# Performance work log

Measured on AMD Instinct MI355X. Metric: run time of the kernel, lower is better.

The kernel has to match this reference:

```python
import jax, jax.numpy as jnp
import numpy as np

D = 1024
H = 16
HD = D // H
LN_EPS = 1e-5
RMS_EPS = 1e-6


def layernorm(x, g, b):
    mu = jnp.mean(x, axis=-1, keepdims=True)
    var = jnp.mean(jnp.square(x - mu), axis=-1, keepdims=True)
    return (x - mu) * jax.lax.rsqrt(var + LN_EPS) * g + b


def rmsnorm(x, w):
    ms = jnp.mean(jnp.square(x), axis=-1, keepdims=True)
    return x * jax.lax.rsqrt(ms + RMS_EPS) * w


def setup_inputs() -> dict:
    key = jax.random.key(0)
    ks = jax.random.split(key, 8)
    s = 0.02
    ones = jnp.ones((D,), jnp.float32)
    zeros = jnp.zeros((D,), jnp.float32)
    return {
        "query_tokens": jax.random.normal(ks[0], (4, 512, D), jnp.float32),
        "point_features": jax.random.normal(ks[1], (4, 4096, D), jnp.float32),
        "ln_q_g": ones, "ln_q_b": zeros,
        "ln_kv_g": ones, "ln_kv_b": zeros,
        "Wq": jax.random.normal(ks[2], (D, D), jnp.float32) * s, "bq": zeros,
        "Wk": jax.random.normal(ks[3], (D, D), jnp.float32) * s, "bk": zeros,
        "Wv": jax.random.normal(ks[4], (D, D), jnp.float32) * s, "bv": zeros,
        "rms_q_w": ones, "rms_k_w": ones,
        "Wo": jax.random.normal(ks[5], (D, D), jnp.float32) * s, "bo": zeros,
        "ln_mlp_g": ones, "ln_mlp_b": zeros,
        "W1": jax.random.normal(ks[6], (D, 4 * D), jnp.float32) * s,
        "b1": jnp.zeros((4 * D,), jnp.float32),
        "W2": jax.random.normal(ks[7], (4 * D, D), jnp.float32) * s,
        "b2": zeros,
    }


def reference(query_tokens, point_features, ln_q_g, ln_q_b, ln_kv_g, ln_kv_b,
              Wq, bq, Wk, bk, Wv, bv, rms_q_w, rms_k_w, Wo, bo,
              ln_mlp_g, ln_mlp_b, W1, b1, W2, b2):
    B, K, _ = query_tokens.shape
    N = point_features.shape[1]
    q_in = layernorm(query_tokens, ln_q_g, ln_q_b)
    kv_in = layernorm(point_features, ln_kv_g, ln_kv_b)
    q = rmsnorm(q_in @ Wq + bq, rms_q_w)          # [B,K,D]
    k = rmsnorm(kv_in @ Wk + bk, rms_k_w)         # [B,N,D]
    v = kv_in @ Wv + bv                            # [B,N,D]
    q = q.reshape(B, K, H, HD)
    k = k.reshape(B, N, H, HD)
    v = v.reshape(B, N, H, HD)
    scores = jnp.einsum('bkhd,bnhd->bhkn', q, k) / jnp.sqrt(jnp.float32(HD))
    attn = jax.nn.softmax(scores, axis=-1)
    ctx = jnp.einsum('bhkn,bnhd->bkhd', attn, v).reshape(B, K, D)
    out = ctx @ Wo + bo + query_tokens
    h = layernorm(out, ln_mlp_g, ln_mlp_b)
    mlp = jax.nn.gelu(h @ W1 + b1, approximate=False) @ W2 + b2
    return out + mlp
```

## Files before the change

### kernel.cpp

```cpp
#include <hip/hip_runtime.h>
#include <math.h>

#define DD   1024
#define NHD  16
#define HDIM 64
#define BB   4
#define QN   512
#define KVN  4096
#define FF   4096

typedef __attribute__((ext_vector_type(8))) short bf16x8;
typedef __attribute__((ext_vector_type(4))) float f32x4;

__device__ __forceinline__ float b2f(ushort u){
  union { unsigned u32; float f; } x; x.u32 = ((unsigned)u)<<16; return x.f;
}
__device__ __forceinline__ ushort f2b(float f){
  unsigned u = __float_as_uint(f);
  unsigned r = (u + 0x7FFFu + ((u>>16)&1u)) >> 16;
  return (ushort)r;
}
__device__ __forceinline__ float ldx(const void* p, size_t i, int isbf){
  return isbf ? b2f(((const ushort*)p)[i]) : ((const float*)p)[i];
}
__device__ __forceinline__ int detect_bf(const void* gref){
  return ((const unsigned*)gref)[0] == 0x3F803F80u;
}

#if defined(__has_builtin)
#if __has_builtin(__builtin_amdgcn_global_load_lds)
#define HAS_GLL 1
#endif
#endif
#ifndef HAS_GLL
#define HAS_GLL 0
#endif
__device__ __forceinline__ void stage16(const ushort* g, ushort* lds_base, int lane){
#if HAS_GLL
  __builtin_amdgcn_global_load_lds(g, lds_base, 16, 0, 0);
#else
  *(uint4*)(lds_base + lane*8) = *(const uint4*)g;
#endif
}

__device__ __forceinline__ void wave_barrier(){
  asm volatile("" ::: "memory");
  __builtin_amdgcn_s_barrier();
  asm volatile("" ::: "memory");
}

__global__ __launch_bounds__(256)
void trans_all(const void* __restrict__ Wq, const void* __restrict__ Wk,
               const void* __restrict__ Wv, const void* __restrict__ Wo,
               const void* __restrict__ W1, const void* __restrict__ W2,
               ushort* __restrict__ WqT, ushort* __restrict__ WkvT,
               ushort* __restrict__ WoT,
               ushort* __restrict__ W1T, ushort* __restrict__ W2T,
               const void* __restrict__ gref)
{
  const int isbf = detect_bf(gref);
  int bid = blockIdx.x;
  const void* src; ushort* dst; int R, C, tid;
  if (bid < 1024){
    int s = bid >> 8; tid = bid & 255; R = 1024; C = 1024;
    src = (s==0) ? Wq : (s==1) ? Wk : (s==2) ? Wv : Wo;
    dst = (s==0) ? WqT : (s==1) ? WkvT : (s==2) ? (WkvT + (size_t)1024*1024) : WoT;
  } else if (bid < 2048){ tid = bid - 1024; src = W1; dst = W1T; R = 1024; C = 4096; }
  else                  { tid = bid - 2048; src = W2; dst = W2T; R = 4096; C = 1024; }
  int ntx = C >> 6;
  int tx = tid % ntx, ty = tid / ntx;
  int r0 = ty*64, c0 = tx*64;

  __shared__ __align__(16) ushort tile[64][72];
  int t = threadIdx.x;
  if (isbf){
    #pragma unroll
    for (int i=0;i<2;i++){
      int idx = t + i*256;
      int r = idx>>3, ch = idx&7;
      #pragma unroll
      for (int j=0;j<8;j++)
        tile[r][ch*8+j] = ((const ushort*)src)[(size_t)(r0+r)*C + c0 + ch*8 + j];
    }
  } else {
    #pragma unroll
    for (int i=0;i<2;i++){
      int idx = t + i*256;
      int r = idx>>3, ch = idx&7;
      const float* s4 = (const float*)src + (size_t)(r0+r)*C + c0 + ch*8;
      float4 f0 = *(const float4*)s4;
      float4 f1 = *(const float4*)(s4+4);
      tile[r][ch*8+0]=f2b(f0.x); tile[r][ch*8+1]=f2b(f0.y);
      tile[r][ch*8+2]=f2b(f0.z); tile[r][ch*8+3]=f2b(f0.w);
      tile[r][ch*8+4]=f2b(f1.x); tile[r][ch*8+5]=f2b(f1.y);
      tile[r][ch*8+6]=f2b(f1.z); tile[r][ch*8+7]=f2b(f1.w);
    }
  }
  __syncthreads();
  #pragma unroll
  for (int i=0;i<2;i++){
    int idx = t + i*256;
    int c = idx>>3, ch = idx&7;
    __align__(16) ushort tmp[8];
    #pragma unroll
    for (int j=0;j<8;j++) tmp[j] = tile[ch*8+j][c];
    *(uint4*)(dst + (size_t)(c0+c)*R + r0 + ch*8) = *(uint4*)tmp;
  }
}

__global__ __launch_bounds__(256)
void ln_all(const void* __restrict__ qtok, const void* __restrict__ pfeat,
            const void* __restrict__ gq, const void* __restrict__ bq,
            const void* __restrict__ gkv, const void* __restrict__ bkv,
            ushort* __restrict__ q_ln, ushort* __restrict__ kv_ln,
            const void* __restrict__ gref)
{
  const int isbf = detect_bf(gref);
  int row = blockIdx.x, t = threadIdx.x;
  const void* src; const void* g; const void* bb; ushort* dst; int r;
  if (row < BB*QN){ src = qtok;  g = gq;  bb = bq;  dst = q_ln;  r = row; }
  else            { src = pfeat; g = gkv; bb = bkv; dst = kv_ln; r = row - BB*QN; }
  int c0 = t*4;
  float v[4];
  if (isbf){
    #pragma unroll
    for (int i=0;i<4;i++) v[i] = b2f(((const ushort*)src)[(size_t)r*DD + c0 + i]);
  } else {
    float4 f = *(const float4*)((const float*)src + (size_t)r*DD + c0);
    v[0]=f.x; v[1]=f.y; v[2]=f.z; v[3]=f.w;
  }
  float s1=0.f, s2=0.f;
  #pragma unroll
  for (int i=0;i<4;i++){ s1 += v[i]; s2 += v[i]*v[i]; }
  #pragma unroll
  for (int off=32; off; off>>=1){ s1 += __shfl_xor(s1,off,64); s2 += __shfl_xor(s2,off,64); }
  __shared__ float r1[4], r2[4];
  int wave = t>>6;
  if ((t&63)==0){ r1[wave]=s1; r2[wave]=s2; }
  __syncthreads();
  s1 = r1[0]+r1[1]+r1[2]+r1[3];
  s2 = r2[0]+r2[1]+r2[2]+r2[3];
  float mu  = s1 * (1.0f/DD);
  float var = s2 * (1.0f/DD) - mu*mu;
  float rs  = rsqrtf(var + 1e-5f);
  union { ushort u[4]; uint2 w; } pk;
  #pragma unroll
  for (int i=0;i<4;i++)
    pk.u[i] = f2b((v[i]-mu)*rs*ldx(g,c0+i,isbf) + ldx(bb,c0+i,isbf));
  *(uint2*)(dst + (size_t)r*DD + c0) = pk.w;
}

__global__ __launch_bounds__(256)
void ln_combine(const float* __restrict__ p0, const float* __restrict__ p1,
                const void* __restrict__ bo, const void* __restrict__ qtok,
                const void* __restrict__ g, const void* __restrict__ bb,
                float* __restrict__ outb, ushort* __restrict__ y,
                const void* __restrict__ gref)
{
  const int isbf = detect_bf(gref);
  int row = blockIdx.x, t = threadIdx.x;
  int c0 = t*4;
  size_t base = (size_t)row*DD + c0;
  float4 a0 = *(const float4*)(p0 + base);
  float4 a1 = *(const float4*)(p1 + base);
  float v[4] = {a0.x+a1.x, a0.y+a1.y, a0.z+a1.z, a0.w+a1.w};
  if (isbf){
    #pragma unroll
    for (int i=0;i<4;i++)
      v[i] += b2f(((const ushort*)qtok)[base+i]) + b2f(((const ushort*)bo)[c0+i]);
  } else {
    float4 q4 = *(const float4*)((const float*)qtok + base);
    v[0] += q4.x + ((const float*)bo)[c0+0];
    v[1] += q4.y + ((const float*)bo)[c0+1];
    v[2] += q4.z + ((const float*)bo)[c0+2];
    v[3] += q4.w + ((const float*)bo)[c0+3];
  }
  float4 ov; ov.x=v[0]; ov.y=v[1]; ov.z=v[2]; ov.w=v[3];
  *(float4*)(outb + base) = ov;

  float s1=0.f, s2=0.f;
  #pragma unroll
  for (int i=0;i<4;i++){ s1 += v[i]; s2 += v[i]*v[i]; }
  #pragma unroll
  for (int off=32; off; off>>=1){ s1 += __shfl_xor(s1,off,64); s2 += __shfl_xor(s2,off,64); }
  __shared__ float r1[4], r2[4];
  int wave = t>>6;
  if ((t&63)==0){ r1[wave]=s1; r2[wave]=s2; }
  __syncthreads();
  s1 = r1[0]+r1[1]+r1[2]+r1[3];
  s2 = r2[0]+r2[1]+r2[2]+r2[3];
  float mu  = s1 * (1.0f/DD);
  float var = s2 * (1.0f/DD) - mu*mu;
  float rs  = rsqrtf(var + 1e-5f);
  union { ushort u[4]; uint2 w; } pk;
  #pragma unroll
  for (int i=0;i<4;i++)
    pk.u[i] = f2b((v[i]-mu)*rs*ldx(g,c0+i,isbf) + ldx(bb,c0+i,isbf));
  *(uint2*)(y + base) = pk.w;
}

__global__ __launch_bounds__(256)
void combine_w2(const float* __restrict__ P0, const float* __restrict__ P1,
                const float* __restrict__ P2, const void* __restrict__ b2,
                const float* __restrict__ res, void* __restrict__ out,
                const void* __restrict__ gref)
{
  const int isbf = detect_bf(gref);
  const size_t PSZ = (size_t)BB*QN*DD;
  size_t i = ((size_t)blockIdx.x*256 + threadIdx.x)*4;
  float4 v = *(const float4*)(P0 + i);
  #pragma unroll
  for (int z=1; z<4; z++){
    float4 p = *(const float4*)(P0 + (size_t)z*PSZ + i);
    v.x+=p.x; v.y+=p.y; v.z+=p.z; v.w+=p.w;
  }
  #pragma unroll
  for (int z=0; z<2; z++){
    float4 p = *(const float4*)(P1 + (size_t)z*PSZ + i);
    v.x+=p.x; v.y+=p.y; v.z+=p.z; v.w+=p.w;
  }
  #pragma unroll
  for (int z=0; z<2; z++){
    float4 p = *(const float4*)(P2 + (size_t)z*PSZ + i);
    v.x+=p.x; v.y+=p.y; v.z+=p.z; v.w+=p.w;
  }
  float4 r = *(const float4*)(res + i);
  int col = (int)(i & (DD-1));
  v.x += r.x + ldx(b2,col+0,isbf);
  v.y += r.y + ldx(b2,col+1,isbf);
  v.z += r.z + ldx(b2,col+2,isbf);
  v.w += r.w + ldx(b2,col+3,isbf);
  if (isbf){
    union { ushort u[4]; uint2 w; } pk;
    pk.u[0]=f2b(v.x); pk.u[1]=f2b(v.y); pk.u[2]=f2b(v.z); pk.u[3]=f2b(v.w);
    *(uint2*)((ushort*)out + i) = pk.w;
  } else {
    *(float4*)((float*)out + i) = v;
  }
}

__global__ __launch_bounds__(256)
void rms_all(ushort* __restrict__ qb, const void* __restrict__ wq,
             ushort* __restrict__ kb, const void* __restrict__ wk,
             const void* __restrict__ gref)
{
  const int isbf = detect_bf(gref);
  int row = blockIdx.x, t = threadIdx.x;
  ushort* x; const void* w; int r;
  if (row < BB*QN){ x = qb; w = wq; r = row; }
  else            { x = kb; w = wk; r = row - BB*QN; }
  int c0 = t*4;
  union { ushort u[4]; uint2 w; } in;
  in.w = *(const uint2*)(x + (size_t)r*DD + c0);
  float v[4];
  #pragma unroll
  for (int i=0;i<4;i++) v[i] = b2f(in.u[i]);
  float s2 = 0.f;
  #pragma unroll
  for (int i=0;i<4;i++) s2 += v[i]*v[i];
  #pragma unroll
  for (int off=32; off; off>>=1) s2 += __shfl_xor(s2,off,64);
  __shared__ float r2[4];
  int wave = t>>6;
  if ((t&63)==0) r2[wave]=s2;
  __syncthreads();
  s2 = r2[0]+r2[1]+r2[2]+r2[3];
  float rs = rsqrtf(s2*(1.0f/DD) + 1e-6f);
  union { ushort u[4]; uint2 w; } pk;
  #pragma unroll
  for (int i=0;i<4;i++) pk.u[i] = f2b(v[i]*rs*ldx(w,c0+i,isbf));
  *(uint2*)(x + (size_t)r*DD + c0) = pk.w;
}

template<int ACT_GELU, int OUT_MODE, int RES_MODE>
__global__ __launch_bounds__(256)
void gemm_bt(const ushort* __restrict__ A, const ushort* __restrict__ BT,
             const void* __restrict__ bias,
             const void* __restrict__ res_ext, const float* __restrict__ res_f,
             void* __restrict__ Cout, void* __restrict__ Cout2,
             int M, int N, int Kdim, int Kstride,
             const void* __restrict__ gref)
{
  const int isbf = detect_bf(gref);
  __shared__ __align__(16) ushort As[128*64];
  __shared__ __align__(16) ushort Bs[128*64];
  const int bm = blockIdx.y * 128;
  const int bn = blockIdx.x * 128;
  const int kz = blockIdx.z;
  const int t = threadIdx.x;
  const int wave = t>>6, lane = t&63, quad = lane>>4, l16 = lane&15;
  const int wm = (wave&1)*64, wn = (wave>>1)*64;

  const ushort* ga[4]; const ushort* gb[4];
  #pragma unroll
  for (int j=0;j<4;j++){
    int row = (t>>3) + j*32;
    int g = ((t&7) - row) & 7;
    ga[j] = A  + (size_t)(bm+row)*Kstride + kz*Kdim + g*8;
    gb[j] = BT + (size_t)(bn+row)*Kstride + kz*Kdim + g*8;
  }

  int offA[2][4], offB[2][4];
  #pragma unroll
  for (int kk=0;kk<2;kk++)
    #pragma unroll
    for (int i=0;i<4;i++){
      int ra = wm + i*16 + l16;
      offA[kk][i] = ra*64 + ((quad + kk*4 + ra)&7)*8;
      int rb = wn + i*16 + l16;
      offB[kk][i] = rb*64 + ((quad + kk*4 + rb)&7)*8;
    }

  f32x4 zero = {0.f,0.f,0.f,0.f};
  f32x4 acc[4][4];
  #pragma unroll
  for (int i=0;i<4;i++)
    #pragma unroll
    for (int j=0;j<4;j++) acc[i][j] = zero;

  const int kiters = Kdim >> 6;
  for (int ki = 0; ki < kiters; ki++) {
    #pragma unroll
    for (int j=0;j<4;j++){
      stage16(ga[j], As + (size_t)(j*256 + wave*64)*8, lane);
      stage16(gb[j], Bs + (size_t)(j*256 + wave*64)*8, lane);
      ga[j] += 64; gb[j] += 64;
    }
    __syncthreads();
    #pragma unroll
    for (int kk=0;kk<2;kk++){
      bf16x8 af[4], bfr[4];
      #pragma unroll
      for (int i=0;i<4;i++){
        af[i]  = *(const bf16x8*)(As + offA[kk][i]);
        bfr[i] = *(const bf16x8*)(Bs + offB[kk][i]);
      }
      #pragma unroll
      for (int mt=0;mt<4;mt++)
        #pragma unroll
        for (int nt=0;nt<4;nt++)
          acc[mt][nt] = __builtin_amdgcn_mfma_f32_16x16x32_bf16(af[mt], bfr[nt], acc[mt][nt], 0,0,0);
    }
    __syncthreads();
  }

  if (OUT_MODE == 4){
    float* P = (float*)Cout + (size_t)kz*M*N;
    #pragma unroll
    for (int mt=0;mt<4;mt++){
      #pragma unroll
      for (int r=0;r<4;r++){
        int row = bm + wm + mt*16 + quad*4 + r;
        #pragma unroll
        for (int nt=0;nt<4;nt++){
          int col = bn + wn + nt*16 + l16;
          P[(size_t)row*N + col] = acc[mt][nt][r];
        }
      }
    }
    return;
  }

  float bv[4];
  #pragma unroll
  for (int nt=0;nt<4;nt++) bv[nt] = ldx(bias, bn + wn + nt*16 + l16, isbf);
  #pragma unroll
  for (int mt=0;mt<4;mt++){
    #pragma unroll
    for (int r=0;r<4;r++){
      int row = bm + wm + mt*16 + quad*4 + r;
      #pragma unroll
      for (int nt=0;nt<4;nt++){
        int col = bn + wn + nt*16 + l16;
        float v = acc[mt][nt][r] + bv[nt];
        if (ACT_GELU) v = 0.5f*v*(1.0f + erff(v*0.70710678118f));
        size_t oi = (size_t)row*N + col;
        if (RES_MODE==1) v += ldx(res_ext, oi, isbf);
        if (RES_MODE==2) v += res_f[oi];
        if (OUT_MODE==0)      ((ushort*)Cout)[oi] = f2b(v);
        else if (OUT_MODE==1) ((float*)Cout)[oi]  = v;
        else { if (isbf) ((ushort*)Cout)[oi] = f2b(v); else ((float*)Cout)[oi] = v; }
      }
    }
  }
}

#define G_HB  32768
#define G_RA0 0
#define G_RA1 8192
#define G_RB0 16384
#define G_RB1 24576

#define G_STAGE(src, R, tile) do{ \
  ushort* _d = ldsb + (((tile)&1)*G_HB + (R) + wave*1024); \
  stage16(src[0] + ((tile)<<6), _d,       lane); \
  stage16(src[1] + ((tile)<<6), _d + 512, lane); \
}while(0)

#define G_LDA(dst, base) \
  _Pragma("unroll") for (int kk=0;kk<2;kk++) \
  _Pragma("unroll") for (int m=0;m<4;m++) \
    dst[kk][m] = *(const bf16x8*)((base) + offA[kk][m]);

#define G_LDB(dst, base) \
  _Pragma("unroll") for (int kk=0;kk<2;kk++) \
  _Pragma("unroll") for (int n=0;n<2;n++) \
    dst[kk][n] = *(const bf16x8*)((base) + offB[kk][n]);

#define G_MM16(ar, br, MO, NO) \
  _Pragma("unroll") for (int kk=0;kk<2;kk++) \
  _Pragma("unroll") for (int m=0;m<4;m++) \
  _Pragma("unroll") for (int n=0;n<2;n++) \
    acc[m+(MO)][n+(NO)] = __builtin_amdgcn_mfma_f32_16x16x32_bf16(ar[kk][m], br[kk][n], acc[m+(MO)][n+(NO)], 0,0,0);

#define G_SYNC() do{ wave_barrier(); \
  asm volatile("s_waitcnt lgkmcnt(0)" ::: "memory"); \
  __builtin_amdgcn_sched_barrier(0); \
  __builtin_amdgcn_s_setprio(1); }while(0)

#define G_END() do{ __builtin_amdgcn_s_setprio(0); wave_barrier(); }while(0)

template<int MODE>
__global__ __launch_bounds__(512, 2)
void gemm256(const ushort* __restrict__ A, const ushort* __restrict__ Aq,
             const ushort* __restrict__ BT, const ushort* __restrict__ BTq,
             const void* __restrict__ biasK, const void* __restrict__ biasV,
             const void* __restrict__ biasQ,
             ushort* __restrict__ Kout, ushort* __restrict__ Vt,
             ushort* __restrict__ Qout,
             float* __restrict__ P0, float* __restrict__ P1,
             float* __restrict__ P2,
             int Kdim, int Kstride,
             const void* __restrict__ gref)
{
  const int isbf = detect_bf(gref);
  __shared__ __align__(16) ushort ldsb[65536];
  const int nb = blockIdx.x;
  int bx, by, kz = 0; bool qmode = false;
  if (MODE == 0){
    int k = nb & 7, j = nb >> 3;
    if (j < 64){ int kvid = 64*k + j; bx = kvid & 7; by = kvid >> 3; }
    else { int qid = 8*k + (j - 64); bx = qid & 7; by = qid >> 3; qmode = true;
           if (bx >= 4) return; }
  } else {
    int wsw = (nb & 7)*32 + (nb >> 3);
    bx = wsw & 3; by = (wsw >> 2) & 7; kz = wsw >> 5;
  }
  const ushort* Ab = (MODE==0 && qmode) ? Aq : A;
  const ushort* Bb = (MODE==0 && qmode) ? BTq : BT;
  const int bmrow = by*256;
  const int bn = bx*256;
  const int koff = (MODE==1) ? kz*Kdim : 0;
  const int t = threadIdx.x;
  const int wave = t>>6, lane = t&63, quad = lane>>4, l16 = lane&15;
  const int wg = wave>>2, wn = wave&3;

  const ushort *sA0[2], *sA1[2], *sB0[2], *sB1[2];
  #pragma unroll
  for (int jj=0;jj<2;jj++){
    int r = (wave*2 + jj)*8 + (lane>>3);
    int g = ((lane&7) - r) & 7;
    int grA0 = r + (r & 64);
    int gc0  = (r & 31) + ((r >> 5) << 6);
    sA0[jj] = Ab + (size_t)(bmrow + grA0     )*Kstride + koff + g*8;
    sA1[jj] = Ab + (size_t)(bmrow + grA0 + 64)*Kstride + koff + g*8;
    sB0[jj] = Bb + (size_t)(bn + gc0      )*Kstride + koff + g*8;
    sB1[jj] = Bb + (size_t)(bn + gc0 + 32 )*Kstride + koff + g*8;
  }

  int offA[2][4], offB[2][2];
  #pragma unroll
  for (int kk=0;kk<2;kk++){
    int slot = ((kk*4 + quad + l16) & 7) * 8;
    #pragma unroll
    for (int m=0;m<4;m++) offA[kk][m] = (wg*64 + m*16 + l16)*64 + slot;
    #pragma unroll
    for (int n=0;n<2;n++) offB[kk][n] = (wn*32 + n*16 + l16)*64 + slot;
  }

  f32x4 zero = {0.f,0.f,0.f,0.f};
  f32x4 acc[8][4];
  #pragma unroll
  for (int i=0;i<8;i++)
    #pragma unroll
    for (int j=0;j<4;j++) acc[i][j] = zero;

  G_STAGE(sA0, G_RA0, 0);
  G_STAGE(sB0, G_RB0, 0);
  G_STAGE(sB1, G_RB1, 0);
  G_STAGE(sA1, G_RA1, 0);
  G_STAGE(sA0, G_RA0, 1);
  G_STAGE(sB1, G_RB1, 1);
  G_STAGE(sA1, G_RA1, 1);
  asm volatile("s_waitcnt vmcnt(6)" ::: "memory");
  wave_barrier();

  const int niter = Kdim >> 7;
  const ushort* L0 = ldsb;
  const ushort* L1 = ldsb + G_HB;
  bf16x8 a[2][4], b[2][2], b1[2][2];

  for (int i = 0; i < niter; ++i) {
    const bool st = (i + 1 < niter);
    G_LDA(a, L0 + G_RA0); G_LDB(b, L0 + G_RB0);
    G_STAGE(sB0, G_RB0, 2*i+1);
    G_SYNC(); G_MM16(a, b, 0, 0); G_END();
    G_LDB(b1, L0 + G_RB1);
    if (st) G_STAGE(sA0, G_RA0, 2*i+2);
    G_SYNC(); G_MM16(a, b1, 0, 2); G_END();
    G_LDA(a, L0 + G_RA1);
    if (st) G_STAGE(sB1, G_RB1, 2*i+2);
    G_SYNC(); G_MM16(a, b1, 4, 2); G_END();
    if (st) G_STAGE(sA1, G_RA1, 2*i+2);
    G_SYNC(); G_MM16(a, b, 4, 0);
    __builtin_amdgcn_s_setprio(0);
    if (st) { asm volatile("s_waitcnt vmcnt(6)" ::: "memory"); }
    else    { asm volatile("s_waitcnt vmcnt(0)" ::: "memory"); }
    wave_barrier();
    G_LDA(a, L1 + G_RA0); G_LDB(b, L1 + G_RB0);
    if (st) G_STAGE(sB0, G_RB0, 2*i+2);
    G_SYNC(); G_MM16(a, b, 0, 0); G_END();
    G_LDB(b1, L1 + G_RB1);
    if (st) G_STAGE(sA0, G_RA0, 2*i+3);
    G_SYNC(); G_MM16(a, b1, 0, 2); G_END();
    G_LDA(a, L1 + G_RA1);
    if (st) G_STAGE(sB1, G_RB1, 2*i+3);
    G_SYNC(); G_MM16(a, b1, 4, 2); G_END();
    if (st) G_STAGE(sA1, G_RA1, 2*i+3);
    G_SYNC(); G_MM16(a, b, 4, 0);
    __builtin_amdgcn_s_setprio(0);
    if (st) { asm volatile("s_waitcnt vmcnt(6)" ::: "memory"); }
    wave_barrier();
  }

  if (MODE == 1){
    const size_t PSZ = (size_t)BB*QN*DD;
    float* P = (kz < 4) ? P0 + (size_t)kz*PSZ
             : (kz < 6) ? P1 + (size_t)(kz-4)*PSZ
                        : P2 + (size_t)(kz-6)*PSZ;
    #pragma unroll
    for (int mt=0;mt<8;mt++){
      #pragma unroll
      for (int r=0;r<4;r++){
        int row = bmrow + wg*128 + mt*16 + quad*4 + r;
        #pragma unroll
        for (int nt=0;nt<4;nt++){
          int col = bn + wn*64 + nt*16 + l16;
          P[(size_t)row*1024 + col] = acc[mt][nt][r];
        }
      }
    }
    return;
  }
  if (qmode){
    float bvv[4];
    #pragma unroll
    for (int nt=0;nt<4;nt++) bvv[nt] = ldx(biasQ, bn + wn*64 + nt*16 + l16, isbf);
    #pragma unroll
    for (int mt=0;mt<8;mt++){
      #pragma unroll
      for (int r=0;r<4;r++){
        int row = bmrow + wg*128 + mt*16 + quad*4 + r;
        #pragma unroll
        for (int nt=0;nt<4;nt++){
          int col = bn + wn*64 + nt*16 + l16;
          Qout[(size_t)row*1024 + col] = f2b(acc[mt][nt][r] + bvv[nt]);
        }
      }
    }
  } else if (bn < 1024){
    float bvv[4];
    #pragma unroll
    for (int nt=0;nt<4;nt++) bvv[nt] = ldx(biasK, bn + wn*64 + nt*16 + l16, isbf);
    #pragma unroll
    for (int mt=0;mt<8;mt++){
      #pragma unroll
      for (int r=0;r<4;r++){
        int row = bmrow + wg*128 + mt*16 + quad*4 + r;
        #pragma unroll
        for (int nt=0;nt<4;nt++){
          int col = bn + wn*64 + nt*16 + l16;
          Kout[(size_t)row*1024 + col] = f2b(acc[mt][nt][r] + bvv[nt]);
        }
      }
    }
  } else {
    float bvv[4];
    #pragma unroll
    for (int nt=0;nt<4;nt++) bvv[nt] = ldx(biasV, bn - 1024 + wn*64 + nt*16 + l16, isbf);
    #pragma unroll
    for (int mt=0;mt<8;mt++){
      int row0 = bmrow + wg*128 + mt*16 + quad*4;
      int bi = row0 >> 12, tok = row0 & (KVN-1);
      #pragma unroll
      for (int nt=0;nt<4;nt++){
        int cl = bn - 1024 + wn*64 + nt*16 + l16;
        union { ushort u[4]; uint2 w2; } pk;
        #pragma unroll
        for (int r=0;r<4;r++) pk.u[r] = f2b(acc[mt][nt][r] + bvv[nt]);
        size_t o = ((size_t)((bi*NHD + (cl>>6))*HDIM + (cl&63)))*KVN + tok;
        *(uint2*)(Vt + o) = pk.w2;
      }
    }
  }
}

__global__ __launch_bounds__(256, 3)
void flash_attn3(const ushort* __restrict__ Q, const ushort* __restrict__ K,
                 const ushort* __restrict__ Vt, float* __restrict__ Op,
                 float* __restrict__ ML)
{
  __shared__ __align__(16) ushort Ks[128*72];
  __shared__ __align__(16) ushort Vs[64*136];
  __shared__ __align__(16) ushort Ps[4][16*136];
  const int bh = blockIdx.x, qt = blockIdx.y, hf = blockIdx.z;
  const int b = bh>>4, h = bh&15;
  const int t = threadIdx.x, wave = t>>6, lane = t&63, quad = lane>>4, l16 = lane&15;
  ushort* Pz = Ps[wave];

  const float QS = 0.125f * 1.4426950408889634f;
  bf16x8 qf[2][2];
  #pragma unroll
  for (int mt=0;mt<2;mt++){
    const ushort* qb = Q + (size_t)(b*QN + qt*128 + wave*32 + mt*16 + l16)*DD + h*HDIM;
    bf16x8 r0 = *(const bf16x8*)(qb + quad*8);
    bf16x8 r1 = *(const bf16x8*)(qb + 32 + quad*8);
    #pragma unroll
    for (int j=0;j<8;j++){
      qf[mt][0][j] = (short)f2b(b2f((ushort)r0[j]) * QS);
      qf[mt][1][j] = (short)f2b(b2f((ushort)r1[j]) * QS);
    }
  }

  f32x4 zero = {0.f,0.f,0.f,0.f};
  f32x4 o[2][4];
  #pragma unroll
  for (int mt=0;mt<2;mt++)
    #pragma unroll
    for (int nt=0;nt<4;nt++) o[mt][nt] = zero;
  float lp[2][4] = {{0.f,0.f,0.f,0.f},{0.f,0.f,0.f,0.f}};

  const ushort* kgb = K  + (size_t)(b*KVN + hf*1024)*DD + h*HDIM;
  const ushort* vtb = Vt + ((size_t)bh*HDIM)*KVN + hf*1024;
  const int kcs = t&7;

  for (int kv0 = 0; kv0 < 1024; kv0 += 128) {
    #pragma unroll
    for (int j=0;j<4;j++){
      int kr = (t>>3) + j*32;
      *(uint4*)(Ks + kr*72 + kcs*8) =
        *(const uint4*)(kgb + (size_t)(kv0+kr)*DD + kcs*8);
    }
    #pragma unroll
    for (int j=0;j<4;j++){
      int p = t + j*256; int vr = p>>4, vc = p&15;
      uint4 d = *(const uint4*)(vtb + (size_t)vr*KVN + kv0 + vc*8);
      ushort* pv = (ushort*)&d;
      ushort* vbp = Vs + vr*136 + (vc&1)*64 + (vc>>1);
      #pragma unroll
      for (int jj=0;jj<8;jj++) vbp[jj*8] = pv[jj];
    }
    __syncthreads();

    f32x4 pb[2][8];
    #pragma unroll
    for (int nt=0;nt<8;nt++){
      const ushort* kb = Ks + (nt*16+l16)*72 + quad*8;
      bf16x8 kf0 = *(const bf16x8*)kb;
      bf16x8 kf1 = *(const bf16x8*)(kb + 32);
      #pragma unroll
      for (int mt=0;mt<2;mt++){
        f32x4 a = __builtin_amdgcn_mfma_f32_16x16x32_bf16(qf[mt][0], kf0, zero, 0,0,0);
        a = __builtin_amdgcn_mfma_f32_16x16x32_bf16(qf[mt][1], kf1, a, 0,0,0);
        #pragma unroll
        for (int r=0;r<4;r++) a[r] = __builtin_amdgcn_exp2f(fminf(a[r], 88.f));
        pb[mt][nt] = a;
      }
    }
    #pragma unroll
    for (int mt=0;mt<2;mt++){
      #pragma unroll
      for (int r=0;r<4;r++){
        float ls = 0.f;
        bf16x8 pk;
        #pragma unroll
        for (int nt=0;nt<8;nt++){
          ls += pb[mt][nt][r];
          pk[nt] = (short)(__float_as_uint(pb[mt][nt][r]) >> 16);
        }
        lp[mt][r] += ls;
        *(bf16x8*)(Pz + (quad*4+r)*136 + l16*8) = pk;
      }
      #pragma unroll
      for (int kc=0;kc<4;kc++){
        bf16x8 pa = *(const bf16x8*)(Pz + l16*136 + kc*32 + quad*8);
        pb[mt][kc] = *(f32x4*)&pa;
      }
    }
    #pragma unroll
    for (int nt=0;nt<4;nt++){
      const ushort* vbr = Vs + (nt*16+l16)*136;
      #pragma unroll
      for (int kc=0;kc<4;kc++){
        bf16x8 vf = *(const bf16x8*)(vbr + kc*32 + quad*8);
        o[0][nt] = __builtin_amdgcn_mfma_f32_16x16x32_bf16(*(bf16x8*)&pb[0][kc], vf, o[0][nt], 0,0,0);
        o[1][nt] = __builtin_amdgcn_mfma_f32_16x16x32_bf16(*(bf16x8*)&pb[1][kc], vf, o[1][nt], 0,0,0);
      }
    }
    __syncthreads();
  }

  const int slot = hf*256 + bh*4 + qt;
  float* Ob = Op + (size_t)slot*128*64;
  #pragma unroll
  for (int mt=0;mt<2;mt++)
    #pragma unroll
    for (int nt=0;nt<4;nt++)
      #pragma unroll
      for (int r=0;r<4;r++)
        Ob[(wave*32 + mt*16 + quad*4 + r)*64 + nt*16 + l16] = o[mt][nt][r];
  #pragma unroll
  for (int mt=0;mt<2;mt++)
    #pragma unroll
    for (int r=0;r<4;r++){
      float v = lp[mt][r];
      #pragma unroll
      for (int off=1; off<16; off<<=1) v += __shfl_xor(v, off, 64);
      if (l16 == 0)
        ML[(size_t)slot*128 + wave*32 + mt*16 + quad*4 + r] = v;
    }
}

__global__ __launch_bounds__(256)
void flash_combine4(const float* __restrict__ Op, const float* __restrict__ ML,
                    ushort* __restrict__ Ctx)
{
  const int bq = blockIdx.x;
  const int bh = bq>>2, qt = bq&3;
  const int b = bh>>4, h = bh&15;
  const int t = threadIdx.x;
  const int row = t>>1, hd0 = (t&1)*32;
  float l = 0.f;
  #pragma unroll
  for (int i=0;i<4;i++) l += ML[(size_t)(i*256 + bq)*128 + row];
  float inv = 1.0f / l;
  float4 a[8];
  #pragma unroll
  for (int c=0;c<8;c++){ a[c].x=0.f; a[c].y=0.f; a[c].z=0.f; a[c].w=0.f; }
  #pragma unroll
  for (int i=0;i<4;i++){
    const float* s = Op + ((size_t)(i*256 + bq)*128 + row)*64 + hd0;
    #pragma unroll
    for (int c=0;c<8;c++){
      float4 v = *(const float4*)(s + c*4);
      a[c].x += v.x; a[c].y += v.y; a[c].z += v.z; a[c].w += v.w;
    }
  }
  ushort* dst = Ctx + (size_t)(b*QN + qt*128 + row)*DD + h*HDIM + hd0;
  #pragma unroll
  for (int c=0;c<8;c++){
    union { ushort u[4]; uint2 w; } pk;
    pk.u[0] = f2b(a[c].x*inv); pk.u[1] = f2b(a[c].y*inv);
    pk.u[2] = f2b(a[c].z*inv); pk.u[3] = f2b(a[c].w*inv);
    *(uint2*)(dst + c*4) = pk.w;
  }
}

extern "C" void kernel_launch(void* const* d_in, const int* in_sizes, int n_in,
                              void* d_out, int out_size, void* d_ws, size_t ws_size,
                              hipStream_t stream)
{
  const void* qtok    = d_in[0];
  const void* pfeat   = d_in[1];
  const void* ln_q_g  = d_in[2];
  const void* ln_q_b  = d_in[3];
  const void* ln_kv_g = d_in[4];
  const void* ln_kv_b = d_in[5];
  const void* Wq      = d_in[6];
  const void* bq      = d_in[7];
  const void* Wk      = d_in[8];
  const void* bk      = d_in[9];
  const void* Wv      = d_in[10];
  const void* bv      = d_in[11];
  const void* rms_q_w = d_in[12];
  const void* rms_k_w = d_in[13];
  const void* Wo      = d_in[14];
  const void* bo      = d_in[15];
  const void* ln_mlp_g= d_in[16];
  const void* ln_mlp_b= d_in[17];
  const void* W1      = d_in[18];
  const void* b1      = d_in[19];
  const void* W2      = d_in[20];
  const void* b2      = d_in[21];
  const void* gref    = ln_q_g;

  char* w = (char*)d_ws;
  auto take = [&](size_t bytes)->char*{ char* p = w; w += (bytes + 255) & ~(size_t)255; return p; };
  ushort* WqT  = (ushort*)take((size_t)DD*DD*2);
  ushort* WkvT = (ushort*)take((size_t)2*DD*DD*2);
  ushort* WoT  = (ushort*)take((size_t)DD*DD*2);
  ushort* W1T  = (ushort*)take((size_t)DD*FF*2);
  ushort* W2T  = (ushort*)take((size_t)FF*DD*2);
  ushort* kv_ln= (ushort*)take((size_t)BB*KVN*DD*2);
  ushort* q_ln = (ushort*)take((size_t)BB*QN*DD*2);
  ushort* kbuf = (ushort*)take((size_t)BB*KVN*DD*2);
  ushort* qbuf = (ushort*)take((size_t)BB*QN*DD*2);
  ushort* Vt   = (ushort*)take((size_t)BB*KVN*DD*2);
  ushort* ctx  = WqT;
  float*  outb = (float*)kbuf;
  ushort* mlp1 = kv_ln;
  float*  Op   = (float*)kv_ln;
  float*  ML   = (float*)q_ln;
  float*  o_parts  = (float*)kv_ln;
  ushort* h_ln = q_ln;
  float*  w2p0 = (float*)Vt;
  float*  w2p1 = (float*)(kv_ln + (size_t)8*1024*1024);
  float*  w2p2 = (float*)d_ws;

  trans_all<<<3072,256,0,stream>>>(Wq,Wk,Wv,Wo,W1,W2, WqT,WkvT,WoT,W1T,W2T, gref);
  ln_all<<<BB*QN + BB*KVN,256,0,stream>>>(qtok,pfeat, ln_q_g,ln_q_b, ln_kv_g,ln_kv_b,
                                          q_ln, kv_ln, gref);
  gemm256<0><<<576, 512, 0, stream>>>(kv_ln, q_ln, WkvT, WqT, bk, bv, bq,
                                      kbuf, Vt, qbuf, nullptr, nullptr, nullptr,
                                      DD, DD, gref);
  rms_all<<<BB*QN + BB*KVN,256,0,stream>>>(qbuf, rms_q_w, kbuf, rms_k_w, gref);
  flash_attn3<<<dim3(64,4,4),256,0,stream>>>(qbuf, kbuf, Vt, Op, ML);
  flash_combine4<<<256,256,0,stream>>>(Op, ML, ctx);
  gemm_bt<0,4,0><<<dim3(8,16,2),256,0,stream>>>(ctx, WoT, nullptr, nullptr,nullptr,
                                                o_parts, nullptr, BB*QN, DD, DD/2, DD, gref);
  ln_combine<<<BB*QN,256,0,stream>>>(o_parts, o_parts + (size_t)BB*QN*DD,
                                     bo, qtok, ln_mlp_g, ln_mlp_b, outb, h_ln, gref);
  gemm_bt<1,0,0><<<dim3(32,16),256,0,stream>>>(h_ln, W1T, b1, nullptr,nullptr,
                                               mlp1, nullptr, BB*QN, FF, DD, DD, gref);
  gemm256<1><<<256, 512, 0, stream>>>(mlp1, nullptr, W2T, nullptr,
                                      nullptr, nullptr, nullptr,
                                      nullptr, nullptr, nullptr,
                                      w2p0, w2p1, w2p2, FF/8, FF, gref);
  combine_w2<<<BB*QN*DD/1024,256,0,stream>>>(w2p0, w2p1, w2p2, b2, outb, d_out, gref);
}
```

Measured before the change: 515.5 us.

## Fuse weight transpose with layernorm, split Q projection out, add MFMA priority hints

Merges the weight-transpose/convert kernel and the input layernorm kernel into one launch. The Q projection moves out of the 256-tile KV GEMM into a separate gemm_bt launch, so the big GEMM no longer carries Q blocks or half-empty early-return tiles. The flash attention loop now raises wave priority around its MFMA calls. This removes one launch and the tail imbalance in the KV GEMM, at the cost of an extra launch for Q that runs serially before the KV GEMM.

```diff
diff --git a/kernel.cpp b/kernel.cpp
--- a/kernel.cpp
+++ b/kernel.cpp
@@ -50,73 +50,73 @@
 }
 
 __global__ __launch_bounds__(256)
-void trans_all(const void* __restrict__ Wq, const void* __restrict__ Wk,
-               const void* __restrict__ Wv, const void* __restrict__ Wo,
-               const void* __restrict__ W1, const void* __restrict__ W2,
-               ushort* __restrict__ WqT, ushort* __restrict__ WkvT,
-               ushort* __restrict__ WoT,
-               ushort* __restrict__ W1T, ushort* __restrict__ W2T,
-               const void* __restrict__ gref)
+void prep_all(const void* __restrict__ Wq, const void* __restrict__ Wk,
+              const void* __restrict__ Wv, const void* __restrict__ Wo,
+              const void* __restrict__ W1, const void* __restrict__ W2,
+              ushort* __restrict__ WqT, ushort* __restrict__ WkvT,
+              ushort* __restrict__ WoT,
+              ushort* __restrict__ W1T, ushort* __restrict__ W2T,
+              const void* __restrict__ qtok, const void* __restrict__ pfeat,
+              const void* __restrict__ gq, const void* __restrict__ bq,
+              const void* __restrict__ gkv, const void* __restrict__ bkv,
+              ushort* __restrict__ q_ln, ushort* __restrict__ kv_ln,
+              const void* __restrict__ gref)
 {
   const int isbf = detect_bf(gref);
-  int bid = blockIdx.x;
-  const void* src; ushort* dst; int R, C, tid;
-  if (bid < 1024){
-    int s = bid >> 8; tid = bid & 255; R = 1024; C = 1024;
-    src = (s==0) ? Wq : (s==1) ? Wk : (s==2) ? Wv : Wo;
-    dst = (s==0) ? WqT : (s==1) ? WkvT : (s==2) ? (WkvT + (size_t)1024*1024) : WoT;
-  } else if (bid < 2048){ tid = bid - 1024; src = W1; dst = W1T; R = 1024; C = 4096; }
-  else                  { tid = bid - 2048; src = W2; dst = W2T; R = 4096; C = 1024; }
-  int ntx = C >> 6;
-  int tx = tid % ntx, ty = tid / ntx;
-  int r0 = ty*64, c0 = tx*64;
-
   __shared__ __align__(16) ushort tile[64][72];
+  __shared__ float r1[4], r2[4];
   int t = threadIdx.x;
-  if (isbf){
+
+  if (blockIdx.x < 3072){
+    int bid = blockIdx.x;
+    const void* src; ushort* dst; int R, C, tid;
+    if (bid < 1024){
+      int s = bid >> 8; tid = bid & 255; R = 1024; C = 1024;
+      src = (s==0) ? Wq : (s==1) ? Wk : (s==2) ? Wv : Wo;
+      dst = (s==0) ? WqT : (s==1) ? WkvT : (s==2) ? (WkvT + (size_t)1024*1024) : WoT;
+    } else if (bid < 2048){ tid = bid - 1024; src = W1; dst = W1T; R = 1024; C = 4096; }
+    else                  { tid = bid - 2048; src = W2; dst = W2T; R = 4096; C = 1024; }
+    int ntx = C >> 6;
+    int tx = tid % ntx, ty = tid / ntx;
+    int r0 = ty*64, c0 = tx*64;
+
+    if (isbf){
+      #pragma unroll
+      for (int i=0;i<2;i++){
+        int idx = t + i*256;
+        int r = idx>>3, ch = idx&7;
+        #pragma unroll
+        for (int j=0;j<8;j++)
+          tile[r][ch*8+j] = ((const ushort*)src)[(size_t)(r0+r)*C + c0 + ch*8 + j];
+      }
+    } else {
+      #pragma unroll
+      for (int i=0;i<2;i++){
+        int idx = t + i*256;
+        int r = idx>>3, ch = idx&7;
+        const float* s4 = (const float*)src + (size_t)(r0+r)*C + c0 + ch*8;
+        float4 f0 = *(const float4*)s4;
+        float4 f1 = *(const float4*)(s4+4);
+        tile[r][ch*8+0]=f2b(f0.x); tile[r][ch*8+1]=f2b(f0.y);
+        tile[r][ch*8+2]=f2b(f0.z); tile[r][ch*8+3]=f2b(f0.w);
+        tile[r][ch*8+4]=f2b(f1.x); tile[r][ch*8+5]=f2b(f1.y);
+        tile[r][ch*8+6]=f2b(f1.z); tile[r][ch*8+7]=f2b(f1.w);
+      }
+    }
+    __syncthreads();
     #pragma unroll
     for (int i=0;i<2;i++){
       int idx = t + i*256;
-      int r = idx>>3, ch = idx&7;
-      #pragma unroll
-      for (int j=0;j<8;j++)
-        tile[r][ch*8+j] = ((const ushort*)src)[(size_t)(r0+r)*C + c0 + ch*8 + j];
-    }
-  } else {
-    #pragma unroll
-    for (int i=0;i<2;i++){
-      int idx = t + i*256;
-      int r = idx>>3, ch = idx&7;
-      const float* s4 = (const float*)src + (size_t)(r0+r)*C + c0 + ch*8;
-      float4 f0 = *(const float4*)s4;
-      float4 f1 = *(const float4*)(s4+4);
-      tile[r][ch*8+0]=f2b(f0.x); tile[r][ch*8+1]=f2b(f0.y);
-      tile[r][ch*8+2]=f2b(f0.z); tile[r][ch*8+3]=f2b(f0.w);
-      tile[r][ch*8+4]=f2b(f1.x); tile[r][ch*8+5]=f2b(f1.y);
-      tile[r][ch*8+6]=f2b(f1.z); tile[r][ch*8+7]=f2b(f1.w);
-    }
-  }
-  __syncthreads();
-  #pragma unroll
-  for (int i=0;i<2;i++){
-    int idx = t + i*256;
-    int c = idx>>3, ch = idx&7;
-    __align__(16) ushort tmp[8];
-    #pragma unroll
-    for (int j=0;j<8;j++) tmp[j] = tile[ch*8+j][c];
-    *(uint4*)(dst + (size_t)(c0+c)*R + r0 + ch*8) = *(uint4*)tmp;
-  }
-}
-
-__global__ __launch_bounds__(256)
-void ln_all(const void* __restrict__ qtok, const void* __restrict__ pfeat,
-            const void* __restrict__ gq, const void* __restrict__ bq,
-            const void* __restrict__ gkv, const void* __restrict__ bkv,
-            ushort* __restrict__ q_ln, ushort* __restrict__ kv_ln,
-            const void* __restrict__ gref)
-{
-  const int isbf = detect_bf(gref);
-  int row = blockIdx.x, t = threadIdx.x;
+      int c = idx>>3, ch = idx&7;
+      __align__(16) ushort tmp[8];
+      #pragma unroll
+      for (int j=0;j<8;j++) tmp[j] = tile[ch*8+j][c];
+      *(uint4*)(dst + (size_t)(c0+c)*R + r0 + ch*8) = *(uint4*)tmp;
+    }
+    return;
+  }
+
+  int row = blockIdx.x - 3072;
   const void* src; const void* g; const void* bb; ushort* dst; int r;
   if (row < BB*QN){ src = qtok;  g = gq;  bb = bq;  dst = q_ln;  r = row; }
   else            { src = pfeat; g = gkv; bb = bkv; dst = kv_ln; r = row - BB*QN; }
@@ -134,7 +134,6 @@
   for (int i=0;i<4;i++){ s1 += v[i]; s2 += v[i]*v[i]; }
   #pragma unroll
   for (int off=32; off; off>>=1){ s1 += __shfl_xor(s1,off,64); s2 += __shfl_xor(s2,off,64); }
-  __shared__ float r1[4], r2[4];
   int wave = t>>6;
   if ((t&63)==0){ r1[wave]=s1; r2[wave]=s2; }
   __syncthreads();
@@ -422,12 +421,9 @@
 
 template<int MODE>
 __global__ __launch_bounds__(512, 2)
-void gemm256(const ushort* __restrict__ A, const ushort* __restrict__ Aq,
-             const ushort* __restrict__ BT, const ushort* __restrict__ BTq,
+void gemm256(const ushort* __restrict__ A, const ushort* __restrict__ BT,
              const void* __restrict__ biasK, const void* __restrict__ biasV,
-             const void* __restrict__ biasQ,
              ushort* __restrict__ Kout, ushort* __restrict__ Vt,
-             ushort* __restrict__ Qout,
              float* __restrict__ P0, float* __restrict__ P1,
              float* __restrict__ P2,
              int Kdim, int Kstride,
@@ -436,18 +432,14 @@
   const int isbf = detect_bf(gref);
   __shared__ __align__(16) ushort ldsb[65536];
   const int nb = blockIdx.x;
-  int bx, by, kz = 0; bool qmode = false;
+  int bx, by, kz = 0;
   if (MODE == 0){
     int k = nb & 7, j = nb >> 3;
-    if (j < 64){ int kvid = 64*k + j; bx = kvid & 7; by = kvid >> 3; }
-    else { int qid = 8*k + (j - 64); bx = qid & 7; by = qid >> 3; qmode = true;
-           if (bx >= 4) return; }
+    int kvid = 64*k + j; bx = kvid & 7; by = kvid >> 3;
   } else {
     int wsw = (nb & 7)*32 + (nb >> 3);
     bx = wsw & 3; by = (wsw >> 2) & 7; kz = wsw >> 5;
   }
-  const ushort* Ab = (MODE==0 && qmode) ? Aq : A;
-  const ushort* Bb = (MODE==0 && qmode) ? BTq : BT;
   const int bmrow = by*256;
   const int bn = bx*256;
   const int koff = (MODE==1) ? kz*Kdim : 0;
@@ -462,10 +454,10 @@
     int g = ((lane&7) - r) & 7;
     int grA0 = r + (r & 64);
     int gc0  = (r & 31) + ((r >> 5) << 6);
-    sA0[jj] = Ab + (size_t)(bmrow + grA0     )*Kstride + koff + g*8;
-    sA1[jj] = Ab + (size_t)(bmrow + grA0 + 64)*Kstride + koff + g*8;
-    sB0[jj] = Bb + (size_t)(bn + gc0      )*Kstride + koff + g*8;
-    sB1[jj] = Bb + (size_t)(bn + gc0 + 32 )*Kstride + koff + g*8;
+    sA0[jj] = A  + (size_t)(bmrow + grA0     )*Kstride + koff + g*8;
+    sA1[jj] = A  + (size_t)(bmrow + grA0 + 64)*Kstride + koff + g*8;
+    sB0[jj] = BT + (size_t)(bn + gc0      )*Kstride + koff + g*8;
+    sB1[jj] = BT + (size_t)(bn + gc0 + 32 )*Kstride + koff + g*8;
   }
 
   int offA[2][4], offB[2][2];
@@ -552,23 +544,7 @@
     }
     return;
   }
-  if (qmode){
-    float bvv[4];
-    #pragma unroll
-    for (int nt=0;nt<4;nt++) bvv[nt] = ldx(biasQ, bn + wn*64 + nt*16 + l16, isbf);
-    #pragma unroll
-    for (int mt=0;mt<8;mt++){
-      #pragma unroll
-      for (int r=0;r<4;r++){
-        int row = bmrow + wg*128 + mt*16 + quad*4 + r;
-        #pragma unroll
-        for (int nt=0;nt<4;nt++){
-          int col = bn + wn*64 + nt*16 + l16;
-          Qout[(size_t)row*1024 + col] = f2b(acc[mt][nt][r] + bvv[nt]);
-        }
-      }
-    }
-  } else if (bn < 1024){
+  if (bn < 1024){
     float bvv[4];
     #pragma unroll
     for (int nt=0;nt<4;nt++) bvv[nt] = ldx(biasK, bn + wn*64 + nt*16 + l16, isbf);
@@ -670,8 +646,10 @@
       bf16x8 kf1 = *(const bf16x8*)(kb + 32);
       #pragma unroll
       for (int mt=0;mt<2;mt++){
+        __builtin_amdgcn_s_setprio(1);
         f32x4 a = __builtin_amdgcn_mfma_f32_16x16x32_bf16(qf[mt][0], kf0, zero, 0,0,0);
         a = __builtin_amdgcn_mfma_f32_16x16x32_bf16(qf[mt][1], kf1, a, 0,0,0);
+        __builtin_amdgcn_s_setprio(0);
         #pragma unroll
         for (int r=0;r<4;r++) a[r] = __builtin_amdgcn_exp2f(fminf(a[r], 88.f));
         pb[mt][nt] = a;
@@ -703,8 +681,10 @@
       #pragma unroll
       for (int kc=0;kc<4;kc++){
         bf16x8 vf = *(const bf16x8*)(vbr + kc*32 + quad*8);
+        __builtin_amdgcn_s_setprio(1);
         o[0][nt] = __builtin_amdgcn_mfma_f32_16x16x32_bf16(*(bf16x8*)&pb[0][kc], vf, o[0][nt], 0,0,0);
         o[1][nt] = __builtin_amdgcn_mfma_f32_16x16x32_bf16(*(bf16x8*)&pb[1][kc], vf, o[1][nt], 0,0,0);
+        __builtin_amdgcn_s_setprio(0);
       }
     }
     __syncthreads();
@@ -817,12 +797,13 @@
   float*  w2p1 = (float*)(kv_ln + (size_t)8*1024*1024);
   float*  w2p2 = (float*)d_ws;
 
-  trans_all<<<3072,256,0,stream>>>(Wq,Wk,Wv,Wo,W1,W2, WqT,WkvT,WoT,W1T,W2T, gref);
-  ln_all<<<BB*QN + BB*KVN,256,0,stream>>>(qtok,pfeat, ln_q_g,ln_q_b, ln_kv_g,ln_kv_b,
-                                          q_ln, kv_ln, gref);
-  gemm256<0><<<576, 512, 0, stream>>>(kv_ln, q_ln, WkvT, WqT, bk, bv, bq,
-                                      kbuf, Vt, qbuf, nullptr, nullptr, nullptr,
-                                      DD, DD, gref);
+  prep_all<<<3072 + BB*QN + BB*KVN,256,0,stream>>>(
+      Wq,Wk,Wv,Wo,W1,W2, WqT,WkvT,WoT,W1T,W2T,
+      qtok,pfeat, ln_q_g,ln_q_b, ln_kv_g,ln_kv_b, q_ln, kv_ln, gref);
+  gemm_bt<0,0,0><<<dim3(8,16), 256,0,stream>>>(q_ln,  WqT, bq, nullptr,nullptr,
+                                               qbuf, nullptr, BB*QN, DD, DD, DD, gref);
+  gemm256<0><<<512, 512, 0, stream>>>(kv_ln, WkvT, bk, bv, kbuf, Vt,
+                                      nullptr, nullptr, nullptr, DD, DD, gref);
   rms_all<<<BB*QN + BB*KVN,256,0,stream>>>(qbuf, rms_q_w, kbuf, rms_k_w, gref);
   flash_attn3<<<dim3(64,4,4),256,0,stream>>>(qbuf, kbuf, Vt, Op, ML);
   flash_combine4<<<256,256,0,stream>>>(Op, ML, ctx);
@@ -832,9 +813,8 @@
                                      bo, qtok, ln_mlp_g, ln_mlp_b, outb, h_ln, gref);
   gemm_bt<1,0,0><<<dim3(32,16),256,0,stream>>>(h_ln, W1T, b1, nullptr,nullptr,
                                                mlp1, nullptr, BB*QN, FF, DD, DD, gref);
-  gemm256<1><<<256, 512, 0, stream>>>(mlp1, nullptr, W2T, nullptr,
-                                      nullptr, nullptr, nullptr,
-                                      nullptr, nullptr, nullptr,
+  gemm256<1><<<256, 512, 0, stream>>>(mlp1, W2T, nullptr, nullptr,
+                                      nullptr, nullptr,
                                       w2p0, w2p1, w2p2, FF/8, FF, gref);
   combine_w2<<<BB*QN*DD/1024,256,0,stream>>>(w2p0, w2p1, w2p2, b2, outb, d_out, gref);
 }
```

New measurement: 492.3 us. -4.5%, faster.
